# Kernel tuning notes

Measured on AMD Instinct MI355X. Metric: run time of the kernel, lower is better.

## Reference

```python
import jax, jax.numpy as jnp
import numpy as np

INPUT_SIZE = 512
OUTPUT_SIZE = 512
BATCH = 65536
HIDDEN = [256, 128, 64, 32]


def _linear_params(key, fan_in, fan_out):
    # torch nn.Linear default init: U(-1/sqrt(fan_in), 1/sqrt(fan_in))
    kw, kb = jax.random.split(key)
    bound = 1.0 / np.sqrt(fan_in)
    w = jax.random.uniform(kw, (fan_out, fan_in), jnp.float32, -bound, bound)
    b = jax.random.uniform(kb, (fan_out,), jnp.float32, -bound, bound)
    return w, b


def setup_inputs() -> dict:
    key = jax.random.key(0)
    ks = jax.random.split(key, 6)
    x = jax.random.normal(ks[0], (BATCH, INPUT_SIZE), jnp.float32)
    dims = [INPUT_SIZE] + HIDDEN + [OUTPUT_SIZE]
    inp = {"x": x}
    for i in range(5):
        w, b = _linear_params(ks[i + 1], dims[i], dims[i + 1])
        inp[f"w{i+1}"] = w
        inp[f"b{i+1}"] = b
    return inp


def reference(x, w1, b1, w2, b2, w3, b3, w4, b4, w5, b5):
    sig = jax.nn.sigmoid
    # in_size = number of nonzero entries in row 0 (replaces per-element python loop)
    in_size = jnp.count_nonzero(x[0])  # traced int scalar
    h = sig(x @ w1.T + b1)
    h = sig(h @ w2.T + b2)
    h = sig(h @ w3.T + b3)
    h = sig(h @ w4.T + b4)
    y = h @ w5.T + b5  # [B, OUTPUT_SIZE]
    # out has shape [B, INPUT_SIZE]; out[:, :in_size] = y[:, :in_size]
    # (INPUT_SIZE == OUTPUT_SIZE here, so a prefix mask suffices)
    mask = jnp.arange(INPUT_SIZE) < in_size  # [INPUT_SIZE]
    out = jnp.where(mask[None, :], y, jnp.zeros((), y.dtype))
    return out
```

## Files before the change

kernel.cpp:

```cpp
#include <hip/hip_runtime.h>
#include <hip/hip_bf16.h>
#include <stdint.h>

typedef __attribute__((ext_vector_type(4))) float f32x4;
typedef __attribute__((ext_vector_type(4))) unsigned int u32x4;
typedef __attribute__((ext_vector_type(8))) short short8;

#define MFMA16(a, b, c) __builtin_amdgcn_mfma_f32_16x16x32_bf16((a), (b), (c), 0, 0, 0)

__device__ __forceinline__ uint16_t f2bf(float f) {
  __hip_bfloat16 h = __float2bfloat16(f);
  return __builtin_bit_cast(uint16_t, h);
}

__device__ __forceinline__ float fast_sigmoid(float v) {
  return __builtin_amdgcn_rcpf(1.f + __expf(-v));
}

__device__ __forceinline__ short8 cvt8(f32x4 a, f32x4 b) {
  short8 r;
  r[0] = (short)f2bf(a[0]); r[1] = (short)f2bf(a[1]);
  r[2] = (short)f2bf(a[2]); r[3] = (short)f2bf(a[3]);
  r[4] = (short)f2bf(b[0]); r[5] = (short)f2bf(b[1]);
  r[6] = (short)f2bf(b[2]); r[7] = (short)f2bf(b[3]);
  return r;
}

__device__ __forceinline__ uint32_t pk2(float a, float b) {
  return (uint32_t)f2bf(a) | ((uint32_t)f2bf(b) << 16);
}

template <int RB>
__device__ __forceinline__ int swzoff(int row, int bcol) {
  constexpr int SLM = (((RB / 16) < 8 ? (RB / 16) : 8)) - 1;
  return row * RB + (bcol ^ ((row & SLM) << 4));
}

template <int RB>
__device__ __forceinline__ short8 lds_a(const uint16_t* buf, int row0, int k0, int lane) {
  int r = row0 + (lane & 15);
  int bcol = (k0 + ((lane >> 4) << 3)) * 2;
  u32x4 raw = *(const u32x4*)((const char*)buf + swzoff<RB>(r, bcol));
  return __builtin_bit_cast(short8, raw);
}

__device__ __forceinline__ short8 load_frag_f32(const float* M, int ld, int r0, int k0, int lane) {
  const float* p = M + (size_t)(r0 + (lane & 15)) * ld + (k0 + ((lane >> 4) << 3));
  f32x4 a = *(const f32x4*)p;
  f32x4 b = *(const f32x4*)(p + 4);
  return cvt8(a, b);
}

__device__ __forceinline__ short8 load_b_pk(const char* base, int f, int lane) {
  u32x4 raw = *(const u32x4*)(base + (((size_t)f * 64 + lane) << 4));
  return __builtin_bit_cast(short8, raw);
}

template <bool P>
__device__ __forceinline__ short8 bfrag(const char* wp, const float* W, int K,
                                        int f0, int ntg, int KT, int kt, int lane) {
  if constexpr (P) {
    return load_b_pk(wp, f0 + ntg * KT + kt, lane);
  } else {
    return load_frag_f32(W, K, ntg * 16, kt * 32, lane);
  }
}

__global__ void pack_kernel(const float* __restrict__ w1, const float* __restrict__ w2,
                            const float* __restrict__ w3, const float* __restrict__ w4,
                            const float* __restrict__ w5, char* __restrict__ ws) {
  int b = blockIdx.x, lane = threadIdx.x;
  const float* W;
  int K, f0;
  if (b < 256)      { W = w1; K = 512; f0 = 0; }
  else if (b < 320) { W = w2; K = 256; f0 = 256; }
  else if (b < 336) { W = w3; K = 128; f0 = 320; }
  else if (b < 340) { W = w4; K = 64;  f0 = 336; }
  else              { W = w5; K = 32;  f0 = 340; }
  int f = b - f0;
  int KT = K / 32;
  int nt = f / KT, kt = f % KT;
  short8 r = load_frag_f32(W, K, nt * 16, kt * 32, lane);
  *(u32x4*)(ws + (((size_t)b * 64 + lane) << 4)) = __builtin_bit_cast(u32x4, r);
}

template <bool P>
__global__ __launch_bounds__(256, 3) void mlp5_kernel(
    const float* __restrict__ x,
    const float* __restrict__ w1, const float* __restrict__ b1,
    const float* __restrict__ w2, const float* __restrict__ b2,
    const float* __restrict__ w3, const float* __restrict__ b3,
    const float* __restrict__ w4, const float* __restrict__ b4,
    const float* __restrict__ w5, const float* __restrict__ b5,
    const char* __restrict__ wp, float* __restrict__ out) {
  __shared__ __align__(16) char smem[32 * 1024];
  uint16_t* XB = (uint16_t*)smem;
  uint16_t* H1 = (uint16_t*)smem;
  uint16_t* H2 = (uint16_t*)smem;
  uint16_t* H3 = (uint16_t*)(smem + 8 * 1024);
  uint16_t* H4 = (uint16_t*)(smem + 12 * 1024);

  const int tid = threadIdx.x;
  const int lane = tid & 63;
  const int wid = tid >> 6;
  const int row0 = blockIdx.x * 32;
  const int lr = (lane >> 4) << 2;
  const int lc = lane & 15;

  const f32x4* xs = (const f32x4*)(x + (size_t)row0 * 512);
  f32x4 xrw[16];
#pragma unroll
  for (int i = 0; i < 16; ++i) xrw[i] = xs[i * 256 + tid];

  short8 bfr[4][4];
#pragma unroll
  for (int nt = 0; nt < 4; ++nt)
    bfr[0][nt] = bfrag<P>(wp, w1, 512, 0, wid * 4 + nt, 16, 0, lane);

  int in_size = 0;
#pragma unroll
  for (int j = 0; j < 8; ++j) {
    float v = x[j * 64 + lane];
    in_size += (int)__popcll(__ballot(v != 0.f));
  }

  const int srow = tid >> 7, scol = (tid & 127) * 8;
#pragma unroll
  for (int i = 0; i < 16; ++i) {
    uint2 w;
    w.x = pk2(xrw[i][0], xrw[i][1]);
    w.y = pk2(xrw[i][2], xrw[i][3]);
    *(uint2*)(smem + swzoff<1024>(2 * i + srow, scol)) = w;
  }
#pragma unroll
  for (int c = 1; c < 4; ++c)
#pragma unroll
    for (int nt = 0; nt < 4; ++nt)
      bfr[c][nt] = bfrag<P>(wp, w1, 512, 0, wid * 4 + nt, 16, c, lane);

  f32x4 acc[2][4];
#pragma unroll
  for (int m = 0; m < 2; ++m)
#pragma unroll
    for (int n = 0; n < 4; ++n) acc[m][n] = (f32x4){0.f, 0.f, 0.f, 0.f};

  __syncthreads();

#pragma unroll
  for (int kt = 0; kt < 16; ++kt) {
    short8 a0 = lds_a<1024>(XB, 0, kt * 32, lane);
    short8 a1 = lds_a<1024>(XB, 16, kt * 32, lane);
#pragma unroll
    for (int nt = 0; nt < 4; ++nt) {
      acc[0][nt] = MFMA16(a0, bfr[kt & 3][nt], acc[0][nt]);
      acc[1][nt] = MFMA16(a1, bfr[kt & 3][nt], acc[1][nt]);
    }
    if (kt + 4 < 16) {
#pragma unroll
      for (int nt = 0; nt < 4; ++nt)
        bfr[kt & 3][nt] = bfrag<P>(wp, w1, 512, 0, wid * 4 + nt, 16, kt + 4, lane);
    }
    __builtin_amdgcn_sched_barrier(0);
  }

  short8 bfr2[2][8];
#pragma unroll
  for (int n = 0; n < 2; ++n)
#pragma unroll
    for (int kt = 0; kt < 8; ++kt)
      bfr2[n][kt] = bfrag<P>(wp, w2, 256, 256, wid * 2 + n, 8, kt, lane);
  float bv1[4];
#pragma unroll
  for (int n = 0; n < 4; ++n) bv1[n] = b1[wid * 64 + n * 16 + lc];

  __syncthreads();

#pragma unroll
  for (int n = 0; n < 4; ++n) {
    const int ncol = wid * 64 + n * 16;
#pragma unroll
    for (int m = 0; m < 2; ++m)
#pragma unroll
      for (int i = 0; i < 4; ++i) {
        float v = fast_sigmoid(acc[m][n][i] + bv1[n]);
        *(uint16_t*)((char*)H1 + swzoff<512>(m * 16 + lr + i, (ncol + lc) * 2)) = f2bf(v);
      }
  }
  __syncthreads();

  {
    f32x4 acc2[2][2];
#pragma unroll
    for (int m = 0; m < 2; ++m)
#pragma unroll
      for (int n = 0; n < 2; ++n) acc2[m][n] = (f32x4){0.f, 0.f, 0.f, 0.f};
#pragma unroll
    for (int m = 0; m < 2; ++m) {
#pragma unroll
      for (int kt = 0; kt < 8; ++kt) {
        short8 afr = lds_a<512>(H1, m * 16, kt * 32, lane);
        acc2[m][0] = MFMA16(afr, bfr2[0][kt], acc2[m][0]);
        acc2[m][1] = MFMA16(afr, bfr2[1][kt], acc2[m][1]);
      }
    }
    short8 bfr3[4];
#pragma unroll
    for (int kt = 0; kt < 4; ++kt)
      bfr3[kt] = bfrag<P>(wp, w3, 128, 320, wid, 4, kt, lane);
    float bv2[2];
#pragma unroll
    for (int n = 0; n < 2; ++n) bv2[n] = b2[wid * 32 + n * 16 + lc];
    __syncthreads();
#pragma unroll
    for (int n = 0; n < 2; ++n) {
      const int ncol = wid * 32 + n * 16;
#pragma unroll
      for (int m = 0; m < 2; ++m)
#pragma unroll
        for (int i = 0; i < 4; ++i) {
          float v = fast_sigmoid(acc2[m][n][i] + bv2[n]);
          *(uint16_t*)((char*)H2 + swzoff<256>(m * 16 + lr + i, (ncol + lc) * 2)) = f2bf(v);
        }
    }
    __syncthreads();

    f32x4 acc3[2];
#pragma unroll
    for (int m = 0; m < 2; ++m) acc3[m] = (f32x4){0.f, 0.f, 0.f, 0.f};
#pragma unroll
    for (int m = 0; m < 2; ++m)
#pragma unroll
      for (int kt = 0; kt < 4; ++kt) {
        short8 afr = lds_a<256>(H2, m * 16, kt * 32, lane);
        acc3[m] = MFMA16(afr, bfr3[kt], acc3[m]);
      }
    short8 bfr4[2];
#pragma unroll
    for (int kt = 0; kt < 2; ++kt)
      bfr4[kt] = bfrag<P>(wp, w4, 64, 336, wid & 1, 2, kt, lane);
    const float bv3 = b3[wid * 16 + lc];
    {
#pragma unroll
      for (int m = 0; m < 2; ++m)
#pragma unroll
        for (int i = 0; i < 4; ++i) {
          float v = fast_sigmoid(acc3[m][i] + bv3);
          *(uint16_t*)((char*)H3 + swzoff<128>(m * 16 + lr + i, (wid * 16 + lc) * 2)) = f2bf(v);
        }
    }
    __syncthreads();

    const int wm = wid >> 1, wn = wid & 1;
    f32x4 acc4 = (f32x4){0.f, 0.f, 0.f, 0.f};
#pragma unroll
    for (int kt = 0; kt < 2; ++kt) {
      short8 afr = lds_a<128>(H3, wm * 16, kt * 32, lane);
      acc4 = MFMA16(afr, bfr4[kt], acc4);
    }
    short8 bfr5[8];
#pragma unroll
    for (int nt = 0; nt < 8; ++nt)
      bfr5[nt] = bfrag<P>(wp, w5, 32, 340, wid * 8 + nt, 1, 0, lane);
    const float bv4 = b4[wn * 16 + lc];
    float bv5[8];
#pragma unroll
    for (int nt = 0; nt < 8; ++nt) bv5[nt] = b5[wid * 128 + nt * 16 + lc];
    {
#pragma unroll
      for (int i = 0; i < 4; ++i) {
        float v = fast_sigmoid(acc4[i] + bv4);
        *(uint16_t*)((char*)H4 + swzoff<64>(wm * 16 + lr + i, (wn * 16 + lc) * 2)) = f2bf(v);
      }
    }
    __syncthreads();

#pragma unroll
    for (int m = 0; m < 2; ++m) {
      short8 afr = lds_a<64>(H4, m * 16, 0, lane);
#pragma unroll
      for (int nt = 0; nt < 8; ++nt) {
        f32x4 av = MFMA16(afr, bfr5[nt], ((f32x4){0.f, 0.f, 0.f, 0.f}));
        const int col = wid * 128 + nt * 16 + lc;
        const bool keep = col < in_size;
#pragma unroll
        for (int i = 0; i < 4; ++i) {
          float v = keep ? (av[i] + bv5[nt]) : 0.f;
          out[(size_t)(row0 + m * 16 + lr + i) * 512 + col] = v;
        }
      }
    }
  }
}

extern "C" void kernel_launch(void* const* d_in, const int* in_sizes, int n_in,
                              void* d_out, int out_size, void* d_ws, size_t ws_size,
                              hipStream_t stream) {
  const float* x  = (const float*)d_in[0];
  const float* w1 = (const float*)d_in[1];
  const float* b1 = (const float*)d_in[2];
  const float* w2 = (const float*)d_in[3];
  const float* b2 = (const float*)d_in[4];
  const float* w3 = (const float*)d_in[5];
  const float* b3 = (const float*)d_in[6];
  const float* w4 = (const float*)d_in[7];
  const float* b4 = (const float*)d_in[8];
  const float* w5 = (const float*)d_in[9];
  const float* b5 = (const float*)d_in[10];
  float* out = (float*)d_out;

  dim3 grid(65536 / 32);
  dim3 block(256);
  const bool packed = ws_size >= (size_t)(372 * 1024);
  if (packed) {
    pack_kernel<<<372, 64, 0, stream>>>(w1, w2, w3, w4, w5, (char*)d_ws);
    mlp5_kernel<true><<<grid, block, 0, stream>>>(x, w1, b1, w2, b2, w3, b3, w4, b4,
                                                  w5, b5, (const char*)d_ws, out);
  } else {
    mlp5_kernel<false><<<grid, block, 0, stream>>>(x, w1, b1, w2, b2, w3, b3, w4, b4,
                                                   w5, b5, nullptr, out);
  }
}
```

Baseline: 73.25 us.

## Split fused MLP into layer-1 kernel and tail kernel via global H1 buffer

```diff
diff --git a/kernel.cpp b/kernel.cpp
--- a/kernel.cpp
+++ b/kernel.cpp
@@ -84,6 +84,232 @@
   *(u32x4*)(ws + (((size_t)b * 64 + lane) << 4)) = __builtin_bit_cast(u32x4, r);
 }
 
+
+__global__ __launch_bounds__(256, 3) void l1_kernel(
+    const float* __restrict__ x, const float* __restrict__ b1,
+    const char* __restrict__ wp, char* __restrict__ h1g) {
+  __shared__ __align__(16) char smem[32 * 1024];
+  uint16_t* XB = (uint16_t*)smem;
+  uint16_t* H1 = (uint16_t*)smem;
+
+  const int tid = threadIdx.x;
+  const int lane = tid & 63;
+  const int wid = tid >> 6;
+  const int row0 = blockIdx.x * 32;
+  const int lr = (lane >> 4) << 2;
+  const int lc = lane & 15;
+
+  const f32x4* xs = (const f32x4*)(x + (size_t)row0 * 512);
+  f32x4 xrw[16];
+#pragma unroll
+  for (int i = 0; i < 16; ++i) xrw[i] = xs[i * 256 + tid];
+
+  short8 bfr[4][4];
+#pragma unroll
+  for (int nt = 0; nt < 4; ++nt)
+    bfr[0][nt] = load_b_pk(wp, (wid * 4 + nt) * 16 + 0, lane);
+
+  const int srow = tid >> 7, scol = (tid & 127) * 8;
+#pragma unroll
+  for (int i = 0; i < 16; ++i) {
+    uint2 w;
+    w.x = pk2(xrw[i][0], xrw[i][1]);
+    w.y = pk2(xrw[i][2], xrw[i][3]);
+    *(uint2*)(smem + swzoff<1024>(2 * i + srow, scol)) = w;
+  }
+#pragma unroll
+  for (int c = 1; c < 4; ++c)
+#pragma unroll
+    for (int nt = 0; nt < 4; ++nt)
+      bfr[c][nt] = load_b_pk(wp, (wid * 4 + nt) * 16 + c, lane);
+
+  f32x4 acc[2][4];
+#pragma unroll
+  for (int m = 0; m < 2; ++m)
+#pragma unroll
+    for (int n = 0; n < 4; ++n) acc[m][n] = (f32x4){0.f, 0.f, 0.f, 0.f};
+
+  __syncthreads();
+
+#pragma unroll
+  for (int kt = 0; kt < 16; ++kt) {
+    short8 a0 = lds_a<1024>(XB, 0, kt * 32, lane);
+    short8 a1 = lds_a<1024>(XB, 16, kt * 32, lane);
+#pragma unroll
+    for (int nt = 0; nt < 4; ++nt) {
+      acc[0][nt] = MFMA16(a0, bfr[kt & 3][nt], acc[0][nt]);
+      acc[1][nt] = MFMA16(a1, bfr[kt & 3][nt], acc[1][nt]);
+    }
+    if (kt + 4 < 16) {
+#pragma unroll
+      for (int nt = 0; nt < 4; ++nt)
+        bfr[kt & 3][nt] = load_b_pk(wp, (wid * 4 + nt) * 16 + kt + 4, lane);
+    }
+    __builtin_amdgcn_sched_barrier(0);
+  }
+
+  float bv1[4];
+#pragma unroll
+  for (int n = 0; n < 4; ++n) bv1[n] = b1[wid * 64 + n * 16 + lc];
+
+  __syncthreads();
+
+#pragma unroll
+  for (int n = 0; n < 4; ++n) {
+    const int ncol = wid * 64 + n * 16;
+#pragma unroll
+    for (int m = 0; m < 2; ++m)
+#pragma unroll
+      for (int i = 0; i < 4; ++i) {
+        float v = fast_sigmoid(acc[m][n][i] + bv1[n]);
+        *(uint16_t*)((char*)H1 + swzoff<512>(m * 16 + lr + i, (ncol + lc) * 2)) = f2bf(v);
+      }
+  }
+  __syncthreads();
+
+  u32x4* dst = (u32x4*)(h1g + (size_t)blockIdx.x * 16384);
+  const u32x4* srcv = (const u32x4*)smem;
+#pragma unroll
+  for (int i = 0; i < 4; ++i) dst[i * 256 + tid] = srcv[i * 256 + tid];
+}
+
+__global__ __launch_bounds__(256, 3) void tail_kernel(
+    const float* __restrict__ x, const char* __restrict__ h1g,
+    const float* __restrict__ b2, const float* __restrict__ b3,
+    const float* __restrict__ b4, const float* __restrict__ b5,
+    const char* __restrict__ wp, float* __restrict__ out) {
+  __shared__ __align__(16) char smem[30 * 1024];
+  uint16_t* H1 = (uint16_t*)smem;
+  uint16_t* H2 = (uint16_t*)(smem + 16 * 1024);
+  uint16_t* H3 = (uint16_t*)(smem + 24 * 1024);
+  uint16_t* H4 = (uint16_t*)(smem + 28 * 1024);
+
+  const int tid = threadIdx.x;
+  const int lane = tid & 63;
+  const int wid = tid >> 6;
+  const int row0 = blockIdx.x * 32;
+  const int lr = (lane >> 4) << 2;
+  const int lc = lane & 15;
+
+  {
+    u32x4* d = (u32x4*)smem;
+    const u32x4* s = (const u32x4*)(h1g + (size_t)blockIdx.x * 16384);
+#pragma unroll
+    for (int i = 0; i < 4; ++i) d[i * 256 + tid] = s[i * 256 + tid];
+  }
+  short8 bfr2[2][8];
+#pragma unroll
+  for (int n = 0; n < 2; ++n)
+#pragma unroll
+    for (int kt = 0; kt < 8; ++kt)
+      bfr2[n][kt] = load_b_pk(wp, 256 + (wid * 2 + n) * 8 + kt, lane);
+
+  int in_size = 0;
+#pragma unroll
+  for (int j = 0; j < 8; ++j) {
+    float v = x[j * 64 + lane];
+    in_size += (int)__popcll(__ballot(v != 0.f));
+  }
+
+  __syncthreads();
+
+  f32x4 acc2[2][2];
+#pragma unroll
+  for (int m = 0; m < 2; ++m)
+#pragma unroll
+    for (int n = 0; n < 2; ++n) acc2[m][n] = (f32x4){0.f, 0.f, 0.f, 0.f};
+#pragma unroll
+  for (int m = 0; m < 2; ++m) {
+#pragma unroll
+    for (int kt = 0; kt < 8; ++kt) {
+      short8 afr = lds_a<512>(H1, m * 16, kt * 32, lane);
+      acc2[m][0] = MFMA16(afr, bfr2[0][kt], acc2[m][0]);
+      acc2[m][1] = MFMA16(afr, bfr2[1][kt], acc2[m][1]);
+    }
+  }
+  short8 bfr3[4];
+#pragma unroll
+  for (int kt = 0; kt < 4; ++kt)
+    bfr3[kt] = load_b_pk(wp, 320 + wid * 4 + kt, lane);
+  float bv2[2];
+#pragma unroll
+  for (int n = 0; n < 2; ++n) bv2[n] = b2[wid * 32 + n * 16 + lc];
+#pragma unroll
+  for (int n = 0; n < 2; ++n) {
+    const int ncol = wid * 32 + n * 16;
+#pragma unroll
+    for (int m = 0; m < 2; ++m)
+#pragma unroll
+      for (int i = 0; i < 4; ++i) {
+        float v = fast_sigmoid(acc2[m][n][i] + bv2[n]);
+        *(uint16_t*)((char*)H2 + swzoff<256>(m * 16 + lr + i, (ncol + lc) * 2)) = f2bf(v);
+      }
+  }
+  __syncthreads();
+
+  f32x4 acc3[2];
+#pragma unroll
+  for (int m = 0; m < 2; ++m) acc3[m] = (f32x4){0.f, 0.f, 0.f, 0.f};
+#pragma unroll
+  for (int m = 0; m < 2; ++m)
+#pragma unroll
+    for (int kt = 0; kt < 4; ++kt) {
+      short8 afr = lds_a<256>(H2, m * 16, kt * 32, lane);
+      acc3[m] = MFMA16(afr, bfr3[kt], acc3[m]);
+    }
+  short8 bfr4[2];
+#pragma unroll
+  for (int kt = 0; kt < 2; ++kt)
+    bfr4[kt] = load_b_pk(wp, 336 + (wid & 1) * 2 + kt, lane);
+  const float bv3 = b3[wid * 16 + lc];
+#pragma unroll
+  for (int m = 0; m < 2; ++m)
+#pragma unroll
+    for (int i = 0; i < 4; ++i) {
+      float v = fast_sigmoid(acc3[m][i] + bv3);
+      *(uint16_t*)((char*)H3 + swzoff<128>(m * 16 + lr + i, (wid * 16 + lc) * 2)) = f2bf(v);
+    }
+  __syncthreads();
+
+  const int wm = wid >> 1, wn = wid & 1;
+  f32x4 acc4 = (f32x4){0.f, 0.f, 0.f, 0.f};
+#pragma unroll
+  for (int kt = 0; kt < 2; ++kt) {
+    short8 afr = lds_a<128>(H3, wm * 16, kt * 32, lane);
+    acc4 = MFMA16(afr, bfr4[kt], acc4);
+  }
+  short8 bfr5[8];
+#pragma unroll
+  for (int nt = 0; nt < 8; ++nt)
+    bfr5[nt] = load_b_pk(wp, 340 + wid * 8 + nt, lane);
+  const float bv4 = b4[wn * 16 + lc];
+  float bv5[8];
+#pragma unroll
+  for (int nt = 0; nt < 8; ++nt) bv5[nt] = b5[wid * 128 + nt * 16 + lc];
+#pragma unroll
+  for (int i = 0; i < 4; ++i) {
+    float v = fast_sigmoid(acc4[i] + bv4);
+    *(uint16_t*)((char*)H4 + swzoff<64>(wm * 16 + lr + i, (wn * 16 + lc) * 2)) = f2bf(v);
+  }
+  __syncthreads();
+
+#pragma unroll
+  for (int m = 0; m < 2; ++m) {
+    short8 afr = lds_a<64>(H4, m * 16, 0, lane);
+#pragma unroll
+    for (int nt = 0; nt < 8; ++nt) {
+      f32x4 av = MFMA16(afr, bfr5[nt], ((f32x4){0.f, 0.f, 0.f, 0.f}));
+      const int col = wid * 128 + nt * 16 + lc;
+      const bool keep = col < in_size;
+#pragma unroll
+      for (int i = 0; i < 4; ++i) {
+        float v = keep ? (av[i] + bv5[nt]) : 0.f;
+        out[(size_t)(row0 + m * 16 + lr + i) * 512 + col] = v;
+      }
+    }
+  }
+}
+
 template <bool P>
 __global__ __launch_bounds__(256, 3) void mlp5_kernel(
     const float* __restrict__ x,
@@ -310,8 +536,17 @@
 
   dim3 grid(65536 / 32);
   dim3 block(256);
+  const size_t H1G_OFF = 512 * 1024;
+  const size_t H1G_BYTES = (size_t)2048 * 16384;
   const bool packed = ws_size >= (size_t)(372 * 1024);
-  if (packed) {
+  const bool split = ws_size >= H1G_OFF + H1G_BYTES;
+  if (split) {
+    pack_kernel<<<372, 64, 0, stream>>>(w1, w2, w3, w4, w5, (char*)d_ws);
+    char* h1g = (char*)d_ws + H1G_OFF;
+    l1_kernel<<<grid, block, 0, stream>>>(x, b1, (const char*)d_ws, h1g);
+    tail_kernel<<<grid, block, 0, stream>>>(x, h1g, b2, b3, b4, b5,
+                                            (const char*)d_ws, out);
+  } else if (packed) {
     pack_kernel<<<372, 64, 0, stream>>>(w1, w2, w3, w4, w5, (char*)d_ws);
     mlp5_kernel<true><<<grid, block, 0, stream>>>(x, w1, b1, w2, b2, w3, b3, w4, b4,
                                                   w5, b5, (const char*)d_ws, out);
```

New measurement: 85.80 us. +17.1%, slower.

## Double rows per block to 64 with 8 waves and separate LDS buffers

Applied to the files above, without the earlier changes.

```diff
diff --git a/kernel.cpp b/kernel.cpp
--- a/kernel.cpp
+++ b/kernel.cpp
@@ -85,7 +85,7 @@
 }
 
 template <bool P>
-__global__ __launch_bounds__(256, 3) void mlp5_kernel(
+__global__ __launch_bounds__(512, 4) void mlp5_kernel(
     const float* __restrict__ x,
     const float* __restrict__ w1, const float* __restrict__ b1,
     const float* __restrict__ w2, const float* __restrict__ b2,
@@ -93,29 +93,29 @@
     const float* __restrict__ w4, const float* __restrict__ b4,
     const float* __restrict__ w5, const float* __restrict__ b5,
     const char* __restrict__ wp, float* __restrict__ out) {
-  __shared__ __align__(16) char smem[32 * 1024];
+  __shared__ __align__(16) char smem[64 * 1024];
   uint16_t* XB = (uint16_t*)smem;
   uint16_t* H1 = (uint16_t*)smem;
-  uint16_t* H2 = (uint16_t*)smem;
-  uint16_t* H3 = (uint16_t*)(smem + 8 * 1024);
-  uint16_t* H4 = (uint16_t*)(smem + 12 * 1024);
+  uint16_t* H2 = (uint16_t*)(smem + 32 * 1024);
+  uint16_t* H3 = (uint16_t*)(smem + 48 * 1024);
+  uint16_t* H4 = (uint16_t*)(smem + 56 * 1024);
 
   const int tid = threadIdx.x;
   const int lane = tid & 63;
   const int wid = tid >> 6;
-  const int row0 = blockIdx.x * 32;
+  const int row0 = blockIdx.x * 64;
   const int lr = (lane >> 4) << 2;
   const int lc = lane & 15;
 
   const f32x4* xs = (const f32x4*)(x + (size_t)row0 * 512);
   f32x4 xrw[16];
 #pragma unroll
-  for (int i = 0; i < 16; ++i) xrw[i] = xs[i * 256 + tid];
-
-  short8 bfr[4][4];
-#pragma unroll
-  for (int nt = 0; nt < 4; ++nt)
-    bfr[0][nt] = bfrag<P>(wp, w1, 512, 0, wid * 4 + nt, 16, 0, lane);
+  for (int i = 0; i < 16; ++i) xrw[i] = xs[i * 512 + tid];
+
+  short8 bfr[4][2];
+#pragma unroll
+  for (int nt = 0; nt < 2; ++nt)
+    bfr[0][nt] = bfrag<P>(wp, w1, 512, 0, wid * 2 + nt, 16, 0, lane);
 
   int in_size = 0;
 #pragma unroll
@@ -130,19 +130,19 @@
     uint2 w;
     w.x = pk2(xrw[i][0], xrw[i][1]);
     w.y = pk2(xrw[i][2], xrw[i][3]);
-    *(uint2*)(smem + swzoff<1024>(2 * i + srow, scol)) = w;
+    *(uint2*)(smem + swzoff<1024>(4 * i + srow, scol)) = w;
   }
 #pragma unroll
   for (int c = 1; c < 4; ++c)
 #pragma unroll
-    for (int nt = 0; nt < 4; ++nt)
-      bfr[c][nt] = bfrag<P>(wp, w1, 512, 0, wid * 4 + nt, 16, c, lane);
-
-  f32x4 acc[2][4];
-#pragma unroll
-  for (int m = 0; m < 2; ++m)
-#pragma unroll
-    for (int n = 0; n < 4; ++n) acc[m][n] = (f32x4){0.f, 0.f, 0.f, 0.f};
+    for (int nt = 0; nt < 2; ++nt)
+      bfr[c][nt] = bfrag<P>(wp, w1, 512, 0, wid * 2 + nt, 16, c, lane);
+
+  f32x4 acc[4][2];
+#pragma unroll
+  for (int m = 0; m < 4; ++m)
+#pragma unroll
+    for (int n = 0; n < 2; ++n) acc[m][n] = (f32x4){0.f, 0.f, 0.f, 0.f};
 
   __syncthreads();
 
@@ -150,36 +150,41 @@
   for (int kt = 0; kt < 16; ++kt) {
     short8 a0 = lds_a<1024>(XB, 0, kt * 32, lane);
     short8 a1 = lds_a<1024>(XB, 16, kt * 32, lane);
-#pragma unroll
-    for (int nt = 0; nt < 4; ++nt) {
+    short8 a2 = lds_a<1024>(XB, 32, kt * 32, lane);
+    short8 a3 = lds_a<1024>(XB, 48, kt * 32, lane);
+#pragma unroll
+    for (int nt = 0; nt < 2; ++nt) {
       acc[0][nt] = MFMA16(a0, bfr[kt & 3][nt], acc[0][nt]);
       acc[1][nt] = MFMA16(a1, bfr[kt & 3][nt], acc[1][nt]);
+      acc[2][nt] = MFMA16(a2, bfr[kt & 3][nt], acc[2][nt]);
+      acc[3][nt] = MFMA16(a3, bfr[kt & 3][nt], acc[3][nt]);
     }
     if (kt + 4 < 16) {
 #pragma unroll
-      for (int nt = 0; nt < 4; ++nt)
-        bfr[kt & 3][nt] = bfrag<P>(wp, w1, 512, 0, wid * 4 + nt, 16, kt + 4, lane);
+      for (int nt = 0; nt < 2; ++nt)
+        bfr[kt & 3][nt] = bfrag<P>(wp, w1, 512, 0, wid * 2 + nt, 16, kt + 4, lane);
     }
     __builtin_amdgcn_sched_barrier(0);
   }
 
+  const int wm2 = wid >> 2, wn2 = wid & 3;
   short8 bfr2[2][8];
 #pragma unroll
   for (int n = 0; n < 2; ++n)
 #pragma unroll
     for (int kt = 0; kt < 8; ++kt)
-      bfr2[n][kt] = bfrag<P>(wp, w2, 256, 256, wid * 2 + n, 8, kt, lane);
-  float bv1[4];
-#pragma unroll
-  for (int n = 0; n < 4; ++n) bv1[n] = b1[wid * 64 + n * 16 + lc];
+      bfr2[n][kt] = bfrag<P>(wp, w2, 256, 256, wn2 * 2 + n, 8, kt, lane);
+  float bv1[2];
+#pragma unroll
+  for (int n = 0; n < 2; ++n) bv1[n] = b1[wid * 32 + n * 16 + lc];
 
   __syncthreads();
 
 #pragma unroll
-  for (int n = 0; n < 4; ++n) {
-    const int ncol = wid * 64 + n * 16;
-#pragma unroll
-    for (int m = 0; m < 2; ++m)
+  for (int n = 0; n < 2; ++n) {
+    const int ncol = wid * 32 + n * 16;
+#pragma unroll
+    for (int m = 0; m < 4; ++m)
 #pragma unroll
       for (int i = 0; i < 4; ++i) {
         float v = fast_sigmoid(acc[m][n][i] + bv1[n]);
@@ -191,101 +196,97 @@
   {
     f32x4 acc2[2][2];
 #pragma unroll
-    for (int m = 0; m < 2; ++m)
-#pragma unroll
-      for (int n = 0; n < 2; ++n) acc2[m][n] = (f32x4){0.f, 0.f, 0.f, 0.f};
-#pragma unroll
-    for (int m = 0; m < 2; ++m) {
+    for (int mt = 0; mt < 2; ++mt)
+#pragma unroll
+      for (int n = 0; n < 2; ++n) acc2[mt][n] = (f32x4){0.f, 0.f, 0.f, 0.f};
+#pragma unroll
+    for (int mt = 0; mt < 2; ++mt) {
 #pragma unroll
       for (int kt = 0; kt < 8; ++kt) {
-        short8 afr = lds_a<512>(H1, m * 16, kt * 32, lane);
-        acc2[m][0] = MFMA16(afr, bfr2[0][kt], acc2[m][0]);
-        acc2[m][1] = MFMA16(afr, bfr2[1][kt], acc2[m][1]);
-      }
-    }
+        short8 afr = lds_a<512>(H1, wm2 * 32 + mt * 16, kt * 32, lane);
+        acc2[mt][0] = MFMA16(afr, bfr2[0][kt], acc2[mt][0]);
+        acc2[mt][1] = MFMA16(afr, bfr2[1][kt], acc2[mt][1]);
+      }
+    }
+    const int wm3 = wid >> 2, wn3 = wid & 3;
     short8 bfr3[4];
 #pragma unroll
     for (int kt = 0; kt < 4; ++kt)
-      bfr3[kt] = bfrag<P>(wp, w3, 128, 320, wid, 4, kt, lane);
+      bfr3[kt] = bfrag<P>(wp, w3, 128, 320, wn3, 4, kt, lane);
     float bv2[2];
 #pragma unroll
-    for (int n = 0; n < 2; ++n) bv2[n] = b2[wid * 32 + n * 16 + lc];
+    for (int n = 0; n < 2; ++n) bv2[n] = b2[wn2 * 32 + n * 16 + lc];
+#pragma unroll
+    for (int n = 0; n < 2; ++n) {
+      const int ncol = wn2 * 32 + n * 16;
+#pragma unroll
+      for (int mt = 0; mt < 2; ++mt)
+#pragma unroll
+        for (int i = 0; i < 4; ++i) {
+          float v = fast_sigmoid(acc2[mt][n][i] + bv2[n]);
+          *(uint16_t*)((char*)H2 + swzoff<256>(wm2 * 32 + mt * 16 + lr + i, (ncol + lc) * 2)) = f2bf(v);
+        }
+    }
     __syncthreads();
-#pragma unroll
-    for (int n = 0; n < 2; ++n) {
-      const int ncol = wid * 32 + n * 16;
-#pragma unroll
-      for (int m = 0; m < 2; ++m)
-#pragma unroll
-        for (int i = 0; i < 4; ++i) {
-          float v = fast_sigmoid(acc2[m][n][i] + bv2[n]);
-          *(uint16_t*)((char*)H2 + swzoff<256>(m * 16 + lr + i, (ncol + lc) * 2)) = f2bf(v);
-        }
-    }
+
+    f32x4 acc3[2];
+#pragma unroll
+    for (int mt = 0; mt < 2; ++mt) acc3[mt] = (f32x4){0.f, 0.f, 0.f, 0.f};
+#pragma unroll
+    for (int mt = 0; mt < 2; ++mt)
+#pragma unroll
+      for (int kt = 0; kt < 4; ++kt) {
+        short8 afr = lds_a<256>(H2, wm3 * 32 + mt * 16, kt * 32, lane);
+        acc3[mt] = MFMA16(afr, bfr3[kt], acc3[mt]);
+      }
+    const int wm4 = wid >> 1, wn4 = wid & 1;
+    short8 bfr4[2];
+#pragma unroll
+    for (int kt = 0; kt < 2; ++kt)
+      bfr4[kt] = bfrag<P>(wp, w4, 64, 336, wn4, 2, kt, lane);
+    const float bv3 = b3[wn3 * 16 + lc];
+#pragma unroll
+    for (int mt = 0; mt < 2; ++mt)
+#pragma unroll
+      for (int i = 0; i < 4; ++i) {
+        float v = fast_sigmoid(acc3[mt][i] + bv3);
+        *(uint16_t*)((char*)H3 + swzoff<128>(wm3 * 32 + mt * 16 + lr + i, (wn3 * 16 + lc) * 2)) = f2bf(v);
+      }
     __syncthreads();
 
-    f32x4 acc3[2];
-#pragma unroll
-    for (int m = 0; m < 2; ++m) acc3[m] = (f32x4){0.f, 0.f, 0.f, 0.f};
-#pragma unroll
-    for (int m = 0; m < 2; ++m)
-#pragma unroll
-      for (int kt = 0; kt < 4; ++kt) {
-        short8 afr = lds_a<256>(H2, m * 16, kt * 32, lane);
-        acc3[m] = MFMA16(afr, bfr3[kt], acc3[m]);
-      }
-    short8 bfr4[2];
-#pragma unroll
-    for (int kt = 0; kt < 2; ++kt)
-      bfr4[kt] = bfrag<P>(wp, w4, 64, 336, wid & 1, 2, kt, lane);
-    const float bv3 = b3[wid * 16 + lc];
-    {
-#pragma unroll
-      for (int m = 0; m < 2; ++m)
-#pragma unroll
-        for (int i = 0; i < 4; ++i) {
-          float v = fast_sigmoid(acc3[m][i] + bv3);
-          *(uint16_t*)((char*)H3 + swzoff<128>(m * 16 + lr + i, (wid * 16 + lc) * 2)) = f2bf(v);
-        }
+    f32x4 acc4 = (f32x4){0.f, 0.f, 0.f, 0.f};
+#pragma unroll
+    for (int kt = 0; kt < 2; ++kt) {
+      short8 afr = lds_a<128>(H3, wm4 * 16, kt * 32, lane);
+      acc4 = MFMA16(afr, bfr4[kt], acc4);
+    }
+    short8 bfr5[4];
+#pragma unroll
+    for (int nt = 0; nt < 4; ++nt)
+      bfr5[nt] = bfrag<P>(wp, w5, 32, 340, wid * 4 + nt, 1, 0, lane);
+    const float bv4 = b4[wn4 * 16 + lc];
+    float bv5[4];
+#pragma unroll
+    for (int nt = 0; nt < 4; ++nt) bv5[nt] = b5[wid * 64 + nt * 16 + lc];
+#pragma unroll
+    for (int i = 0; i < 4; ++i) {
+      float v = fast_sigmoid(acc4[i] + bv4);
+      *(uint16_t*)((char*)H4 + swzoff<64>(wm4 * 16 + lr + i, (wn4 * 16 + lc) * 2)) = f2bf(v);
     }
     __syncthreads();
 
-    const int wm = wid >> 1, wn = wid & 1;
-    f32x4 acc4 = (f32x4){0.f, 0.f, 0.f, 0.f};
-#pragma unroll
-    for (int kt = 0; kt < 2; ++kt) {
-      short8 afr = lds_a<128>(H3, wm * 16, kt * 32, lane);
-      acc4 = MFMA16(afr, bfr4[kt], acc4);
-    }
-    short8 bfr5[8];
-#pragma unroll
-    for (int nt = 0; nt < 8; ++nt)
-      bfr5[nt] = bfrag<P>(wp, w5, 32, 340, wid * 8 + nt, 1, 0, lane);
-    const float bv4 = b4[wn * 16 + lc];
-    float bv5[8];
-#pragma unroll
-    for (int nt = 0; nt < 8; ++nt) bv5[nt] = b5[wid * 128 + nt * 16 + lc];
-    {
-#pragma unroll
-      for (int i = 0; i < 4; ++i) {
-        float v = fast_sigmoid(acc4[i] + bv4);
-        *(uint16_t*)((char*)H4 + swzoff<64>(wm * 16 + lr + i, (wn * 16 + lc) * 2)) = f2bf(v);
-      }
-    }
-    __syncthreads();
-
-#pragma unroll
-    for (int m = 0; m < 2; ++m) {
-      short8 afr = lds_a<64>(H4, m * 16, 0, lane);
-#pragma unroll
-      for (int nt = 0; nt < 8; ++nt) {
+#pragma unroll
+    for (int mt = 0; mt < 4; ++mt) {
+      short8 afr = lds_a<64>(H4, mt * 16, 0, lane);
+#pragma unroll
+      for (int nt = 0; nt < 4; ++nt) {
         f32x4 av = MFMA16(afr, bfr5[nt], ((f32x4){0.f, 0.f, 0.f, 0.f}));
-        const int col = wid * 128 + nt * 16 + lc;
+        const int col = wid * 64 + nt * 16 + lc;
         const bool keep = col < in_size;
 #pragma unroll
         for (int i = 0; i < 4; ++i) {
           float v = keep ? (av[i] + bv5[nt]) : 0.f;
-          out[(size_t)(row0 + m * 16 + lr + i) * 512 + col] = v;
+          out[(size_t)(row0 + mt * 16 + lr + i) * 512 + col] = v;
         }
       }
     }
@@ -308,8 +309,8 @@
   const float* b5 = (const float*)d_in[10];
   float* out = (float*)d_out;
 
-  dim3 grid(65536 / 32);
-  dim3 block(256);
+  dim3 grid(65536 / 64);
+  dim3 block(512);
   const bool packed = ws_size >= (size_t)(372 * 1024);
   if (packed) {
     pack_kernel<<<372, 64, 0, stream>>>(w1, w2, w3, w4, w5, (char*)d_ws);
```

Result: slower. 76.97 us (+5.1%).
